# Kernel optimization log

Measured on AMD Instinct MI355X. Metric: run time of the kernel, lower is better.

The kernel has to match this reference:

```python
import jax, jax.numpy as jnp
import numpy as np
import math

D1 = D2 = D3 = 256
B, S = 2, 384
SCALE = math.sqrt((D1 + D2 + D3) / 3)  # arc_norm scale


def setup_inputs() -> dict:
    key = jax.random.key(0)
    k1, k2, k3, kw = jax.random.split(key, 4)
    matrix_1 = jax.random.normal(k1, (B, S, D1), dtype=jnp.float32)
    matrix_2 = jax.random.normal(k2, (B, S, D2), dtype=jnp.float32)
    matrix_3 = jax.random.normal(k3, (B, S, D3), dtype=jnp.float32)
    # xavier-uniform-like scale for the trilinear tensor parameter
    W = jax.random.normal(kw, (D1, D2, D3), dtype=jnp.float32) * 0.02
    return {"matrix_1": matrix_1, "matrix_2": matrix_2, "matrix_3": matrix_3, "W": W}


def reference(matrix_1, matrix_2, matrix_3, W):
    _, s, _ = matrix_1.shape
    # mode == 'sib': upper-triangular (diag=1) mask over the (j, k) dims
    mask = jnp.triu(jnp.ones((s, s), dtype=bool), k=1)[None, None, :, :]  # [1,1,S,S]
    # Faithful reproduction of the original einsum chain (note: subscripts are
    # exactly as in the torch module, including the independent sum indices).
    v1U = jnp.einsum('bix,pqr->biqr', matrix_1, W)          # [B,S,D2,D3]
    v1Uv2 = jnp.einsum('biqr,bjx->bijr', v1U, matrix_2)      # [B,S,S,D3]
    scores = jnp.einsum('bkx,bijr->bijk', matrix_3, v1Uv2)   # [B,S,S,S]
    scores = jnp.where(mask, scores, 0.0)                    # masked_fill(~mask, 0)
    return scores / SCALE                                    # activation = Passthrough
```

## Files before the change

### kernel.cpp

```cpp
#include <hip/hip_runtime.h>

#define SS 384
#define BB 2
#define DD 256
#define NPART 1024
#define SLAB4 (SS * SS / 4)

typedef float f32x4 __attribute__((ext_vector_type(4)));

#define WS_PART 16
#define WS_M1 2048
#define WS_M2 2816
#define WS_M3 3584

__global__ void stage1_kernel(const float* __restrict__ m1,
                              const float* __restrict__ m2,
                              const float* __restrict__ m3,
                              const float* __restrict__ W,
                              float* __restrict__ ws) {
    if (blockIdx.x < NPART) {
        __shared__ float sm[4];
        const f32x4* W4 = (const f32x4*)W;
        const unsigned n4 = (DD * DD * DD) / 4;
        float s = 0.f;
        for (unsigned i = blockIdx.x * blockDim.x + threadIdx.x; i < n4; i += NPART * 256) {
            f32x4 v = W4[i];
            s += (v.x + v.y) + (v.z + v.w);
        }
        #pragma unroll
        for (int off = 32; off; off >>= 1) s += __shfl_down(s, off, 64);
        int lane = threadIdx.x & 63, w = threadIdx.x >> 6;
        if (lane == 0) sm[w] = s;
        __syncthreads();
        if (threadIdx.x == 0) ws[WS_PART + blockIdx.x] = (sm[0] + sm[1]) + (sm[2] + sm[3]);
    } else {
        int wave = (int)(blockIdx.x - NPART) * 4 + (int)(threadIdx.x >> 6);
        int lane = threadIdx.x & 63;
        if (wave >= 3 * BB * SS) return;
        const float* src;
        float* dst;
        if (wave < BB * SS)          { src = m1 + (size_t)wave * DD;                 dst = ws + WS_M1 + wave; }
        else if (wave < 2 * BB * SS) { src = m2 + (size_t)(wave - BB * SS) * DD;     dst = ws + WS_M2 + (wave - BB * SS); }
        else                         { src = m3 + (size_t)(wave - 2 * BB * SS) * DD; dst = ws + WS_M3 + (wave - 2 * BB * SS); }
        f32x4 v = ((const f32x4*)src)[lane];
        float s = (v.x + v.y) + (v.z + v.w);
        #pragma unroll
        for (int off = 32; off; off >>= 1) s += __shfl_down(s, off, 64);
        if (lane == 0) *dst = s;
    }
}

__global__ void __launch_bounds__(256) writer_kernel(const float* __restrict__ ws,
                                                     float* __restrict__ out) {
    __shared__ float sred[8];
    __shared__ float c1l[BB * SS];
    int t = threadIdx.x;

    const float* p = ws + WS_PART;
    float s = (p[t] + p[t + 256]) + (p[t + 512] + p[t + 768]);
    #pragma unroll
    for (int off = 32; off; off >>= 1) s += __shfl_down(s, off, 64);
    int lane = t & 63, w = t >> 6;
    if (lane == 0) sred[w] = s;
    __syncthreads();
    if (t == 0) sred[4] = (((sred[0] + sred[1]) + (sred[2] + sred[3]))) * (1.0f / 16.0f);
    __syncthreads();
    float wt16 = sred[4];

    c1l[t]       = ws[WS_M1 + t]       * wt16;
    c1l[t + 256] = ws[WS_M1 + t + 256] * wt16;
    c1l[t + 512] = ws[WS_M1 + t + 512] * wt16;

    unsigned g     = blockIdx.x * 256u + t;
    unsigned which = g / SLAB4;
    unsigned so    = g - which * SLAB4;
    int j  = (int)(so / 96);
    int k4 = (int)(so - (unsigned)j * 96);
    int k0 = k4 * 4;

    f32x4 fa = ((const f32x4*)(ws + WS_M3))[k4];
    f32x4 fb = ((const f32x4*)(ws + WS_M3 + SS))[k4];
    f32x4 fm0, fm1;
    fm0.x = (k0 + 0 > j) ? fa.x : 0.f;
    fm0.y = (k0 + 1 > j) ? fa.y : 0.f;
    fm0.z = (k0 + 2 > j) ? fa.z : 0.f;
    fm0.w = (k0 + 3 > j) ? fa.w : 0.f;
    fm1.x = (k0 + 0 > j) ? fb.x : 0.f;
    fm1.y = (k0 + 1 > j) ? fb.y : 0.f;
    fm1.z = (k0 + 2 > j) ? fb.z : 0.f;
    fm1.w = (k0 + 3 > j) ? fb.w : 0.f;
    float m2v0 = ws[WS_M2 + j];
    float m2v1 = ws[WS_M2 + SS + j];
    __syncthreads();

    const float* c1p = c1l + which;
    f32x4* dst = (f32x4*)out + so + (size_t)which * SLAB4;
    #pragma unroll
    for (int ch = 0; ch < 6; ++ch) {
        float m2v = (ch < 3) ? m2v0 : m2v1;
        f32x4 fm  = (ch < 3) ? fm0 : fm1;
        float cj[16];
        #pragma unroll
        for (int q = 0; q < 16; ++q)
            cj[q] = c1p[(ch * 16 + q) * 8] * m2v;
        #pragma unroll
        for (int q = 0; q < 16; ++q) {
            f32x4 o;
            o.x = cj[q] * fm.x;
            o.y = cj[q] * fm.y;
            o.z = cj[q] * fm.z;
            o.w = cj[q] * fm.w;
            dst[(size_t)(ch * 16 + q) * 8 * SLAB4] = o;
        }
    }
}

extern "C" void kernel_launch(void* const* d_in, const int* in_sizes, int n_in,
                              void* d_out, int out_size, void* d_ws, size_t ws_size,
                              hipStream_t stream) {
    const float* m1 = (const float*)d_in[0];
    const float* m2 = (const float*)d_in[1];
    const float* m3 = (const float*)d_in[2];
    const float* W  = (const float*)d_in[3];
    float* out = (float*)d_out;
    float* ws  = (float*)d_ws;

    stage1_kernel<<<NPART + 576, 256, 0, stream>>>(m1, m2, m3, W, ws);
    writer_kernel<<<1152, 256, 0, stream>>>(ws, out);
}
```

Measured before the change: 102.7 us.

## Write fully-masked zero tiles during the W reduction; writer skips them

The first kernel gets extra blocks that store zeros to every float4 of the output that lies entirely below the j<k mask, so these stores run alongside the memory-bound reduction over W. The writer kernel now returns early for those positions and only computes the partially or fully unmasked float4s. Its grid doubles, and each thread covers fewer batch-row slices (12x4 instead of 16x6). The aim is to take roughly half of the output store traffic off the serial path after the reduction. Total bytes written stay the same, so any gain depends on how well the two bandwidth-bound streams share HBM.

```diff
diff --git a/kernel.cpp b/kernel.cpp
--- a/kernel.cpp
+++ b/kernel.cpp
@@ -6,6 +6,10 @@
 #define NPART 1024
 #define SLAB4 (SS * SS / 4)
 
+#define ZBLKS 1152
+#define WBLKS 1024
+#define RBLKS 576
+
 typedef float f32x4 __attribute__((ext_vector_type(4)));
 
 #define WS_PART 16
@@ -13,29 +17,48 @@
 #define WS_M2 2816
 #define WS_M3 3584
 
-__global__ void stage1_kernel(const float* __restrict__ m1,
-                              const float* __restrict__ m2,
-                              const float* __restrict__ m3,
-                              const float* __restrict__ W,
-                              float* __restrict__ ws) {
-    if (blockIdx.x < NPART) {
+__global__ void __launch_bounds__(256) stage1_kernel(const float* __restrict__ m1,
+                                                     const float* __restrict__ m2,
+                                                     const float* __restrict__ m3,
+                                                     const float* __restrict__ W,
+                                                     float* __restrict__ ws,
+                                                     float* __restrict__ out) {
+    int bx = blockIdx.x;
+    int t  = threadIdx.x;
+    if (bx < ZBLKS) {
+        unsigned g     = (unsigned)bx * 256u + (unsigned)t;
+        unsigned which = g / SLAB4;
+        unsigned so    = g - which * SLAB4;
+        int j  = (int)(so / 96);
+        int k4 = (int)(so - (unsigned)j * 96);
+        if (k4 * 4 + 3 <= j) {
+            f32x4 z = {0.f, 0.f, 0.f, 0.f};
+            f32x4* dst = (f32x4*)out + so + (size_t)which * SLAB4;
+            #pragma unroll 8
+            for (int bi = (int)which; bi < BB * SS; bi += 8) {
+                *dst = z;
+                dst += 8 * SLAB4;
+            }
+        }
+    } else if (bx < ZBLKS + WBLKS) {
         __shared__ float sm[4];
+        int wb = bx - ZBLKS;
         const f32x4* W4 = (const f32x4*)W;
         const unsigned n4 = (DD * DD * DD) / 4;
         float s = 0.f;
-        for (unsigned i = blockIdx.x * blockDim.x + threadIdx.x; i < n4; i += NPART * 256) {
+        for (unsigned i = (unsigned)wb * 256u + t; i < n4; i += WBLKS * 256) {
             f32x4 v = W4[i];
             s += (v.x + v.y) + (v.z + v.w);
         }
         #pragma unroll
         for (int off = 32; off; off >>= 1) s += __shfl_down(s, off, 64);
-        int lane = threadIdx.x & 63, w = threadIdx.x >> 6;
+        int lane = t & 63, w = t >> 6;
         if (lane == 0) sm[w] = s;
         __syncthreads();
-        if (threadIdx.x == 0) ws[WS_PART + blockIdx.x] = (sm[0] + sm[1]) + (sm[2] + sm[3]);
+        if (t == 0) ws[WS_PART + wb] = (sm[0] + sm[1]) + (sm[2] + sm[3]);
     } else {
-        int wave = (int)(blockIdx.x - NPART) * 4 + (int)(threadIdx.x >> 6);
-        int lane = threadIdx.x & 63;
+        int wave = (bx - ZBLKS - WBLKS) * 4 + (t >> 6);
+        int lane = t & 63;
         if (wave >= 3 * BB * SS) return;
         const float* src;
         float* dst;
@@ -70,13 +93,15 @@
     c1l[t]       = ws[WS_M1 + t]       * wt16;
     c1l[t + 256] = ws[WS_M1 + t + 256] * wt16;
     c1l[t + 512] = ws[WS_M1 + t + 512] * wt16;
+    __syncthreads();
 
-    unsigned g     = blockIdx.x * 256u + t;
+    unsigned g     = blockIdx.x * 256u + (unsigned)t;
     unsigned which = g / SLAB4;
     unsigned so    = g - which * SLAB4;
     int j  = (int)(so / 96);
     int k4 = (int)(so - (unsigned)j * 96);
     int k0 = k4 * 4;
+    if (k0 + 3 <= j) return;
 
     f32x4 fa = ((const f32x4*)(ws + WS_M3))[k4];
     f32x4 fb = ((const f32x4*)(ws + WS_M3 + SS))[k4];
@@ -91,26 +116,25 @@
     fm1.w = (k0 + 3 > j) ? fb.w : 0.f;
     float m2v0 = ws[WS_M2 + j];
     float m2v1 = ws[WS_M2 + SS + j];
-    __syncthreads();
 
     const float* c1p = c1l + which;
     f32x4* dst = (f32x4*)out + so + (size_t)which * SLAB4;
     #pragma unroll
-    for (int ch = 0; ch < 6; ++ch) {
-        float m2v = (ch < 3) ? m2v0 : m2v1;
-        f32x4 fm  = (ch < 3) ? fm0 : fm1;
-        float cj[16];
+    for (int ch = 0; ch < 4; ++ch) {
+        float m2v = (ch < 2) ? m2v0 : m2v1;
+        f32x4 fm  = (ch < 2) ? fm0 : fm1;
+        float cj[12];
         #pragma unroll
-        for (int q = 0; q < 16; ++q)
-            cj[q] = c1p[(ch * 16 + q) * 8] * m2v;
+        for (int q = 0; q < 12; ++q)
+            cj[q] = c1p[(ch * 12 + q) * 16] * m2v;
         #pragma unroll
-        for (int q = 0; q < 16; ++q) {
+        for (int q = 0; q < 12; ++q) {
             f32x4 o;
             o.x = cj[q] * fm.x;
             o.y = cj[q] * fm.y;
             o.z = cj[q] * fm.z;
             o.w = cj[q] * fm.w;
-            dst[(size_t)(ch * 16 + q) * 8 * SLAB4] = o;
+            dst[(size_t)(ch * 12 + q) * 16 * SLAB4] = o;
         }
     }
 }
@@ -125,6 +149,6 @@
     float* out = (float*)d_out;
     float* ws  = (float*)d_ws;
 
-    stage1_kernel<<<NPART + 576, 256, 0, stream>>>(m1, m2, m3, W, ws);
-    writer_kernel<<<1152, 256, 0, stream>>>(ws, out);
+    stage1_kernel<<<ZBLKS + WBLKS + RBLKS, 256, 0, stream>>>(m1, m2, m3, W, ws, out);
+    writer_kernel<<<2304, 256, 0, stream>>>(ws, out);
 }
```

New measurement: 146.7 us. +42.8%, slower.
